# Kernel optimization log

Hardware: AMD Instinct MI355X
Metric: run time of the kernel (lower is better)

Reference implementation:

```python
import jax, jax.numpy as jnp
import numpy as np
from jax import lax

B, N, FIN, T, K, FC, FT = 8, 2048, 3, 12, 3, 64, 64


def _conv2d(x, w, b, pad):
    # x [B,C,N,T], w [O,I,1,kw], NCHW conv
    y = lax.conv_general_dilated(x, w, (1, 1), pad,
                                 dimension_numbers=('NCHW', 'OIHW', 'NCHW'))
    return y + b[None, :, None, None]


def _spatial_att(h, W, a, alpha, concat):
    # GAT-style dense attention. h [B,N,Fin], W [Fin,D], a [2D,1]
    D = W.shape[1]
    Wh = h @ W                                             # [B,N,D]
    e = jax.nn.leaky_relu(Wh @ a[:D] + jnp.swapaxes(Wh @ a[D:], 1, 2), alpha)  # [B,N,N]
    att = jax.nn.softmax(jax.nn.sigmoid(e), axis=1)        # softmax over dim=1 (as in torch)
    hp = jnp.einsum('bij,bjd->bid', att, Wh)
    return jax.nn.elu(hp) if concat else hp


def setup_inputs() -> dict:
    key = jax.random.key(0)
    ks = jax.random.split(key, 24)
    rnd = lambda i, shape, scale=1.0: (jax.random.normal(ks[i], shape, dtype=jnp.float32) * scale)
    FTm = FC * T  # 768 spatial-attention feature dim
    D = FTm // 2
    return {
        'x': rnd(0, (B, N, FIN, T)),
        'cheb': rnd(1, (K, N, N), 1.0 / np.sqrt(N)),
        'Gamma': rnd(2, (K, FIN, FC), 1.0 / np.sqrt(FIN)),
        'W_heads': rnd(3, (2, FTm, D), 1.0 / np.sqrt(FTm)),
        'a_heads': rnd(4, (2, 2 * D, 1), 1.0 / np.sqrt(2 * D)),
        'W_out': rnd(5, (FTm, FTm), 1.0 / np.sqrt(FTm)),
        'a_out': rnd(6, (2 * FTm, 1), 1.0 / np.sqrt(2 * FTm)),
        'U1': rnd(7, (FT, FT), 1.0 / np.sqrt(FT)),
        'U2': rnd(8, (FT,), 1.0 / np.sqrt(FT)),
        'U3': rnd(9, (FT,), 1.0 / np.sqrt(FT)),
        'be': rnd(10, (1, T, T), 0.1),
        'Ve': rnd(11, (T, T), 1.0 / np.sqrt(T)),
        'time_w': rnd(12, (FT, FC, 1, 3), 1.0 / np.sqrt(3 * FC)),
        'time_b': rnd(13, (FT,), 0.01),
        'res_w': rnd(14, (FT, FIN, 1, 1), 1.0 / np.sqrt(FIN)),
        'res_b': rnd(15, (FT,), 0.01),
        'back_w': rnd(16, (FT, FC, 1, 3), 1.0 / np.sqrt(3 * FC)),
        'back_b': rnd(17, (FT,), 0.01),
        'fore_w': rnd(18, (FT, FC, 1, 3), 1.0 / np.sqrt(3 * FC)),
        'fore_b': rnd(19, (FT,), 0.01),
        'ln_g': jnp.ones((FT,), jnp.float32),
        'ln_b': jnp.zeros((FT,), jnp.float32),
    }


def reference(x, cheb, Gamma, W_heads, a_heads, W_out, a_out, U1, U2, U3, be, Ve,
              time_w, time_b, res_w, res_b, back_w, back_b, fore_w, fore_b, ln_g, ln_b):
    b, n, fin, t = x.shape
    k_ = cheb.shape[0]
    fc = Gamma.shape[2]
    # ChebNetII interpolation coefficients T_k(x_j), x_j = cos((j+0.5)pi/K) -> [j,k]
    jj = np.arange(k_)
    cxj = jnp.asarray(np.cos(np.outer((jj + 0.5) * np.pi / k_, np.arange(k_))), x.dtype)
    lhs = jnp.einsum('jio,jk->kio', Gamma, cxj)                         # [K,Fin,Fc]
    rhs = jnp.einsum('bnit,knm->kbmit', x, cheb)                        # [K,B,N,Fin,T]
    spatial_gcn = jax.nn.relu((2.0 / (k_ + 1)) * jnp.einsum('kbmit,kio->bmot', rhs, lhs))  # [B,N,Fc,T]

    # Spatial transformer: 2 GAT heads + output attention
    h = spatial_gcn.reshape(b, n, fc * t)
    heads = jax.vmap(lambda W, a: _spatial_att(h, W, a, 0.1, True))(W_heads, a_heads)  # [H,B,N,D]
    hcat = jnp.transpose(heads, (1, 2, 0, 3)).reshape(b, n, -1)
    gcn_SAt = jax.nn.relu(_spatial_att(hcat, W_out, a_out, 0.1, False)).reshape(b, n, fc, t)

    # Temporal conv (1x3, pad 1)
    tc = _conv2d(jnp.transpose(gcn_SAt, (0, 2, 1, 3)), time_w, time_b, ((0, 0), (1, 1)))
    tc = jnp.transpose(tc, (0, 2, 1, 3))                                # [B,N,Ft,T]

    # Temporal attention
    lhs_t = jnp.einsum('bnft,fg,g->btn', tc, U1, U2)                    # [B,T,N]
    rhs_t = jnp.einsum('f,bnft->bnt', U3, tc)                           # [B,N,T]
    prod = jnp.einsum('bsn,bnt->bst', lhs_t, rhs_t)                     # [B,T,T]
    E = jnp.einsum('is,bst->bit', Ve, jax.nn.sigmoid(prod + be))
    E = jax.nn.softmax(E, axis=1)
    tcn = jnp.einsum('bnft,bts->bnfs', tc, E)                           # [B,N,Ft,T]

    # Residual (1x1 conv) + LayerNorm over channel dim
    x_res = _conv2d(jnp.transpose(x, (0, 2, 1, 3)), res_w, res_b, ((0, 0), (0, 0)))
    x_res = jnp.transpose(x_res, (0, 2, 1, 3))                          # [B,N,Ft,T]
    z = jnp.transpose(jax.nn.relu(x_res + tcn), (0, 3, 1, 2))           # [B,T,N,Ft]
    mu = z.mean(-1, keepdims=True)
    var = z.var(-1, keepdims=True)
    z = (z - mu) / jnp.sqrt(var + 1e-5) * ln_g + ln_b
    result = jnp.transpose(z, (0, 2, 3, 1))                             # [B,N,Ft,T]

    rp = jnp.transpose(result, (0, 2, 1, 3))
    backcast = jnp.transpose(_conv2d(rp, back_w, back_b, ((0, 0), (1, 1))), (0, 2, 1, 3))
    forecast = jnp.transpose(_conv2d(rp, fore_w, fore_b, ((0, 0), (1, 1))), (0, 2, 1, 3))
    return (backcast, forecast)
```

## Files before the change

kernel.cpp:

```cpp
#include <hip/hip_runtime.h>


typedef unsigned short u16;
typedef __bf16 bf16x8 __attribute__((ext_vector_type(8)));
typedef float f32x4 __attribute__((ext_vector_type(4)));
typedef u16 u16x8 __attribute__((ext_vector_type(8)));

__device__ __forceinline__ u16 f2b(float f) {
  union { float f; unsigned u; } v; v.f = f;
  unsigned u = v.u;
  u = u + 0x7FFFu + ((u >> 16) & 1u);
  return (u16)(u >> 16);
}
__device__ __forceinline__ float b2f(u16 h) {
  union { unsigned u; float f; } v; v.u = ((unsigned)h) << 16; return v.f;
}
__device__ __forceinline__ float qfun(float x) {
  float e = x > 0.f ? x : 0.1f * x;
  float s = __builtin_amdgcn_rcpf(1.f + __expf(-e));
  return __expf(s);
}

#define GLOAD16(g, l) __builtin_amdgcn_global_load_lds( \
    (__attribute__((address_space(1))) void*)(g),       \
    (__attribute__((address_space(3))) void*)(l), 16, 0, 0)

constexpr size_t OFF_LHS     = 0x0;
constexpr size_t OFF_U1U2    = 0x1000;
constexpr size_t OFF_BIASBIG = 0x1100;
constexpr size_t OFF_FH      = 0x3000;
constexpr size_t OFF_GH      = 0x23000;
constexpr size_t OFF_RDH     = 0x43000;
constexpr size_t OFF_FO      = 0x63000;
constexpr size_t OFF_GO      = 0x73000;
constexpr size_t OFF_RDO     = 0x83000;
constexpr size_t OFF_LHST    = 0x93000;
constexpr size_t OFF_RHST    = 0x153000;
constexpr size_t OFF_PROD    = 0x213000;
constexpr size_t OFF_E       = 0x215000;
constexpr size_t OFF_WCATT   = 0x220000;
constexpr size_t OFF_WOUTT   = 0x340000;
constexpr size_t OFF_WTBIG   = 0x460000;
constexpr size_t OFF_XCOLT   = 0x580000;
constexpr size_t OFF_CHEBT   = 0x700000;
constexpr size_t OFF_C1      = 0x1F00000;
constexpr size_t OFF_H       = 0x4300000;
constexpr size_t OFF_P       = 0x700000;
constexpr size_t OFF_WHCATT  = 0x5B00000;
constexpr size_t OFF_HCAT    = 0x7300000;
constexpr size_t OFF_WHOUTT  = 0x5B00000;
constexpr size_t OFF_GCNB    = 0x7300000;
constexpr size_t OFF_WBFBIG  = 0x8B00000;
constexpr size_t OFF_TCS     = 0x700000;
constexpr size_t OFF_RESULTB = 0x3700000;
constexpr size_t WS_NEEDED   = 0x8D40000;

struct GemmP {
  const u16* A; const u16* BT;
  long sA, sB;
  int K, lda, ldb;
  int swz, splitK;
  float* Cf; long sCf; int ldcf;
  u16* Cb;  long sCb; int ldcb;
  u16* CbT; int ldcT; long sCbT;
  const float* bias;
  float* outB; float* outF;
};

template <int EPI>
__global__ __launch_bounds__(256, 2) void gemm_bf16(GemmP p) {
  constexpr int SMEM_U16 = (EPI == 1) ? 17408 : 16384;
  __shared__ u16 smem[SMEM_U16];
  const int tid  = threadIdx.x;
  const int lane = tid & 63;
  const int wid  = tid >> 6;
  const int wm = wid >> 1, wn = wid & 1;
  const int z = blockIdx.z;

  long m0, n0;
  if (p.swz) {
    int nT = gridDim.x;
    int nwg = nT * gridDim.y;
    int lin = blockIdx.x + nT * blockIdx.y;
    int q = nwg >> 3;
    int swz = (lin & 7) * q + (lin >> 3);
    m0 = (long)(swz / nT) * 128;
    n0 = (long)(swz % nT) * 128;
  } else {
    m0 = (long)blockIdx.x * 128;
    n0 = (long)blockIdx.y * 128;
  }

  const int K = p.K;
  long aBase, bBase;
  if (p.splitK) {
    int kz = z >> 2, ch = z & 3;
    aBase = (long)kz * p.sA + (long)ch * 512;
    bBase = (long)ch * 512;
  } else {
    aBase = (long)z * p.sA;
    bBase = (long)z * p.sB;
  }
  const u16* Ab = p.A + aBase + m0 * p.lda;
  const u16* Bb = p.BT + bBase + n0 * p.ldb;

  const int srow = wid * 32 + (lane >> 2);
  const int sk   = (((lane & 3) ^ ((lane >> 3) & 3))) * 8;
  const u16* aP0 = Ab + (long)srow * p.lda + sk;
  const u16* aP1 = aP0 + (long)16 * p.lda;
  const u16* bP0 = Bb + (long)srow * p.ldb + sk;
  const u16* bP1 = bP0 + (long)16 * p.ldb;

  f32x4 acc[4][4];
  f32x4 zero = {0.f, 0.f, 0.f, 0.f};
#pragma unroll
  for (int i = 0; i < 4; ++i)
#pragma unroll
    for (int j = 0; j < 4; ++j) acc[i][j] = zero;

  const int xorc = (lane >> 1) & 3;
  const int aoff = (wm * 64 + (lane & 15)) * 32 + (((lane >> 4) ^ xorc)) * 8;
  const int boff = (wn * 64 + (lane & 15)) * 32 + (((lane >> 4) ^ xorc)) * 8;

  const int lslot = (wid * 2) * 512;

#define STAGE(s, bufbase) do {                                  \
    GLOAD16(aP0 + (long)(s) * 32, (bufbase) + lslot);           \
    GLOAD16(aP1 + (long)(s) * 32, (bufbase) + lslot + 512);     \
    GLOAD16(bP0 + (long)(s) * 32, (bufbase) + 4096 + lslot);    \
    GLOAD16(bP1 + (long)(s) * 32, (bufbase) + 4096 + lslot + 512); } while (0)

  const int nsteps = K >> 5;
  u16* buf0 = smem;
  u16* buf1 = smem + 8192;

  STAGE(0, buf0);
  if (nsteps > 1) {
    STAGE(1, buf1);
    asm volatile("s_waitcnt vmcnt(4)" ::: "memory");
  } else {
    asm volatile("s_waitcnt vmcnt(0)" ::: "memory");
  }
  asm volatile("s_barrier" ::: "memory");

  for (int i = 0; i < nsteps; ++i) {
    const u16* As = smem + (i & 1) * 8192;
    const u16* Bs = As + 4096;
    bf16x8 av[4], bv[4];
#pragma unroll
    for (int mi = 0; mi < 4; ++mi) av[mi] = *(const bf16x8*)&As[aoff + mi * 512];
#pragma unroll
    for (int ni = 0; ni < 4; ++ni) bv[ni] = *(const bf16x8*)&Bs[boff + ni * 512];
#pragma unroll
    for (int mi = 0; mi < 4; ++mi)
#pragma unroll
      for (int ni = 0; ni < 4; ++ni)
        acc[mi][ni] = __builtin_amdgcn_mfma_f32_16x16x32_bf16(av[mi], bv[ni], acc[mi][ni], 0, 0, 0);
    if (i + 1 < nsteps) {
      asm volatile("s_waitcnt lgkmcnt(0)" ::: "memory");
      asm volatile("s_barrier" ::: "memory");
      if (i + 2 < nsteps) {
        STAGE(i + 2, (i & 1) ? buf1 : buf0);
        asm volatile("s_waitcnt vmcnt(4)" ::: "memory");
      } else {
        asm volatile("s_waitcnt vmcnt(0)" ::: "memory");
      }
      asm volatile("s_barrier" ::: "memory");
    }
  }
#undef STAGE
  __syncthreads();

  if constexpr (EPI == 1) {
#pragma unroll
    for (int mi = 0; mi < 4; ++mi)
#pragma unroll
      for (int ni = 0; ni < 4; ++ni) {
        int cl = wn * 64 + ni * 16 + (lane & 15);
        int mlb = wm * 64 + mi * 16 + ((lane >> 4) << 2);
#pragma unroll
        for (int r = 0; r < 4; ++r)
          smem[cl * 136 + mlb + r] = f2b(acc[mi][ni][r]);
      }
    __syncthreads();
    int c = tid >> 1, half = tid & 1;
    long bat = m0 >> 11;
    u16* dst = p.CbT + bat * p.sCbT + (long)(n0 + c) * p.ldcT + (m0 & 2047) + half * 64;
    const u16* srcp = &smem[c * 136 + half * 64];
#pragma unroll
    for (int j = 0; j < 64; j += 8)
      *(u16x8*)(dst + j) = *(const u16x8*)(srcp + j);
    return;
  }

#pragma unroll
  for (int mi = 0; mi < 4; ++mi) {
    long rb0 = m0 + wm * 64 + mi * 16 + ((lane >> 4) << 2);
#pragma unroll
    for (int ni = 0; ni < 4; ++ni) {
      int col = (int)n0 + wn * 64 + ni * 16 + (lane & 15);
#pragma unroll
      for (int r = 0; r < 4; ++r) {
        float v = acc[mi][ni][r];
        long row = rb0 + r;
        if constexpr (EPI == 0) {
          p.Cf[(long)z * p.sCf + row * p.ldcf + col] = v;
        } else if constexpr (EPI == 2) {
          float e = v > 0.f ? v : expm1f(v);
          p.Cb[(long)z * p.sCb + row * p.ldcb + col] = f2b(e);
        } else if constexpr (EPI == 6) {
          p.Cb[row * 768 + col] = f2b(v + p.bias[col & 63]);
        } else if constexpr (EPI == 7) {
          float vb = v + p.bias[col];
          if (col < 768) p.outB[row * 768 + col] = vb;
          else           p.outF[row * 768 + (col - 768)] = vb;
        } else {
          p.Cb[(long)z * p.sCb + row * p.ldcb + col] = f2b(fmaxf(v, 0.f));
        }
      }
    }
  }
}

__global__ void k_prep(const float* Gamma, const float* U1, const float* U2,
                       const float* back_b, const float* fore_b,
                       float* lhs, float* u1u2, float* biasBig) {
  int o = threadIdx.x;
  if (o < 64) {
    const float cx[3][3] = {{1.f, 0.86602540378443871f, 0.5f},
                            {1.f, 6.123233995736766e-17f, -1.f},
                            {1.f, -0.86602540378443871f, 0.5f}};
    for (int k = 0; k < 3; ++k)
      for (int i = 0; i < 3; ++i) {
        float s = 0;
        for (int j = 0; j < 3; ++j) s += Gamma[(j * 3 + i) * 64 + o] * cx[j][k];
        lhs[(k * 3 + i) * 64 + o] = s;
      }
    float s = 0;
    for (int g = 0; g < 64; ++g) s += U1[o * 64 + g] * U2[g];
    u1u2[o] = s;
    for (int t = 0; t < 12; ++t) {
      biasBig[o * 12 + t] = back_b[o];
      biasBig[768 + o * 12 + t] = fore_b[o];
    }
  }
}

__global__ void k_convert(const float* W_heads, const float* W_out, const float* time_w,
                          const float* back_w, const float* fore_w, const float* xg,
                          u16* WcatT, u16* WoutT, u16* WtBig, u16* WbfBig, u16* xcolT) {
  const int N1 = 589824, NT = 589824, NBF = 1179648, N5 = 786432;
  const int TOT = 2 * N1 + NT + NBF + N5;
  for (int o = blockIdx.x * 256 + threadIdx.x; o < TOT; o += gridDim.x * 256) {
    if (o < N1) {
      int dcol = o / 768, kk = o % 768;
      int hd = dcol / 384, d = dcol % 384;
      WcatT[o] = f2b(W_heads[((long)hd * 768 + kk) * 384 + d]);
    } else if (o < 2 * N1) {
      int o2 = o - N1; int dcol = o2 / 768, kk = o2 % 768;
      WoutT[o2] = f2b(W_out[kk * 768 + dcol]);
    } else if (o < 2 * N1 + NT) {
      int o3 = o - 2 * N1; int col = o3 / 768, kk = o3 % 768;
      int t = col >> 6, ft = col & 63, fc = kk / 12, tau = kk % 12;
      int r = tau - t + 1;
      WtBig[o3] = f2b((r >= 0 && r < 3) ? time_w[ft * 192 + fc * 3 + r] : 0.f);
    } else if (o < 2 * N1 + NT + NBF) {
      int o4 = o - 2 * N1 - NT; int col = o4 / 768, kk = o4 % 768;
      int rem = (col < 768) ? col : col - 768;
      int c = rem / 12, tt = rem % 12;
      int fc = kk / 12, tau = kk % 12; int r = tau - tt + 1;
      const float* wsrc = (col < 768) ? back_w : fore_w;
      WbfBig[o4] = f2b((r >= 0 && r < 3) ? wsrc[c * 192 + fc * 3 + r] : 0.f);
    } else {
      int o5 = o - 2 * N1 - NT - NBF; int c = o5 / 2048, n = o5 % 2048;
      float v = 0.f;
      if (c < 288) {
        int b = c / 36, r2 = c % 36, i = r2 / 12, t = r2 % 12;
        v = xg[(long)(b * 2048 + n) * 36 + i * 12 + t];
      }
      xcolT[o5] = f2b(v);
    }
  }
}

__global__ void k_chebT(const float* cheb, u16* chebT) {
  __shared__ float ts[32][33];
  int n0 = blockIdx.x * 32, m0 = blockIdx.y * 32, k = blockIdx.z;
  int c = threadIdx.x & 31, rq = threadIdx.x >> 5;
  const long base = (long)k * 2048 * 2048;
  for (int q = 0; q < 4; ++q) {
    int n = n0 + rq + q * 8;
    ts[rq + q * 8][c] = cheb[base + (long)n * 2048 + m0 + c];
  }
  __syncthreads();
  for (int q = 0; q < 4; ++q) {
    int m = m0 + rq + q * 8;
    chebT[base + (long)m * 2048 + n0 + c] = f2b(ts[c][rq + q * 8]);
  }
}

__global__ __launch_bounds__(256) void k_h(const float* C1, const float* lhs, u16* h) {
  int bn = blockIdx.x; int b = bn >> 11, n = bn & 2047;
  int tid = threadIdx.x;
  __shared__ float c1s[108], ls[576];
  if (tid < 108) {
    int kk = tid / 12, t = tid % 12; int k = kk / 3, i = kk % 3;
    float s = 0;
#pragma unroll
    for (int ch = 0; ch < 4; ++ch)
      s += C1[((long)(k * 4 + ch) * 2048 + n) * 384 + b * 36 + i * 12 + t];
    c1s[tid] = s;
  }
  for (int s = tid; s < 576; s += 256) ls[s] = lhs[s];
  __syncthreads();
  for (int q = 0; q < 3; ++q) {
    int idx = tid + q * 256; int o = idx / 12, t = idx % 12;
    float s = 0;
#pragma unroll
    for (int kk = 0; kk < 9; ++kk) s += c1s[kk * 12 + t] * ls[kk * 64 + o];
    s *= 0.5f;
    if (s < 0.f) s = 0.f;
    h[(long)bn * 768 + idx] = f2b(s);
  }
}

__global__ __launch_bounds__(256) void k_fg(const u16* WhT, int dOff, int Dlen,
                                            const float* aF, const float* aG,
                                            float* fOut, float* gOut) {
  int b = blockIdx.y;
  int i = blockIdx.x * 256 + threadIdx.x;
  __shared__ float af[768], ag[768];
  for (int s = threadIdx.x; s < Dlen; s += 256) { af[s] = aF[s]; ag[s] = aG[s]; }
  __syncthreads();
  const u16* wp = WhT + ((long)b * 768 + dOff) * 2048 + i;
  float fs = 0, gs = 0;
  for (int d = 0; d < Dlen; ++d) {
    float w = b2f(wp[(long)d * 2048]);
    fs += w * af[d]; gs += w * ag[d];
  }
  fOut[b * 2048 + i] = fs;
  gOut[b * 2048 + i] = gs;
}

__global__ __launch_bounds__(256) void k_denom(const float* f, const float* g, float* rd) {
  int b = blockIdx.y;
  int jl = threadIdx.x & 63, ch = threadIdx.x >> 6;
  int j = blockIdx.x * 64 + jl;
  __shared__ float fl[2048];
  __shared__ float red[256];
  for (int s = threadIdx.x; s < 2048; s += 256) fl[s] = f[b * 2048 + s];
  __syncthreads();
  float gj = g[b * 2048 + j];
  float acc = 0;
  for (int i = ch * 512; i < ch * 512 + 512; ++i) acc += qfun(fl[i] + gj);
  red[threadIdx.x] = acc;
  __syncthreads();
  if (ch == 0) {
    float s = red[jl] + red[jl + 64] + red[jl + 128] + red[jl + 192];
    rd[b * 2048 + j] = 1.f / s;
  }
}

__global__ __launch_bounds__(256) void k_P(const float* f, const float* g,
                                           const float* rd, u16* P) {
  int j = blockIdx.x * 256 + threadIdx.x;
  int i0 = blockIdx.y * 16;
  int b = blockIdx.z;
  __shared__ float fl[16];
  if (threadIdx.x < 16) fl[threadIdx.x] = f[b * 2048 + i0 + threadIdx.x];
  __syncthreads();
  float gj = g[b * 2048 + j], rj = rd[b * 2048 + j];
  u16* Pp = P + ((long)b * 2048 + i0) * 2048 + j;
#pragma unroll
  for (int ii = 0; ii < 16; ++ii) Pp[(long)ii * 2048] = f2b(qfun(fl[ii] + gj) * rj);
}

__global__ void k_temporal(const u16* tc, const float* u1u2, const float* U3g,
                           float* lhs_t, float* rhs_t) {
  __shared__ float uu[64], u3[64];
  int tid = threadIdx.x;
  if (tid < 64) { uu[tid] = u1u2[tid]; u3[tid] = U3g[tid]; }
  __syncthreads();
  int gid = blockIdx.x * 256 + tid;
  const u16* p = tc + (long)gid * 64;
  float s1 = 0, s2 = 0;
#pragma unroll
  for (int c = 0; c < 8; ++c) {
    u16x8 vv = *(const u16x8*)(p + c * 8);
#pragma unroll
    for (int j = 0; j < 8; ++j) {
      float v = b2f(vv[j]);
      s1 += v * uu[c * 8 + j]; s2 += v * u3[c * 8 + j];
    }
  }
  int t = gid % 12; long bn = gid / 12;
  int b = (int)(bn >> 11);
  lhs_t[((long)b * 12 + t) * 2048 + (int)(bn & 2047)] = s1;
  rhs_t[gid] = s2;
}

__global__ void k_prod(const float* lhs_t, const float* rhs_t, float* prod) {
  int bi = blockIdx.x;
  int b = bi / 144; int r = bi % 144; int s = r / 12; int u = r % 12;
  int tid = threadIdx.x;
  float acc = 0;
  const float* lp = lhs_t + ((long)b * 12 + s) * 2048;
  const float* rp = rhs_t + (long)b * 2048 * 12 + u;
  for (int n = tid; n < 2048; n += 256) acc += lp[n] * rp[n * 12];
  __shared__ float red[256];
  red[tid] = acc; __syncthreads();
  for (int st = 128; st > 0; st >>= 1) {
    if (tid < st) red[tid] += red[tid + st];
    __syncthreads();
  }
  if (tid == 0) prod[bi] = red[0];
}

__global__ void k_E(const float* prod, const float* be, const float* Ve, float* E) {
  int b = blockIdx.x; int tid = threadIdx.x;
  __shared__ float S0[144], E1[144], mx[12], dn[12];
  if (tid < 144) {
    float v = prod[b * 144 + tid] + be[tid];
    S0[tid] = 1.f / (1.f + __expf(-v));
  }
  __syncthreads();
  if (tid < 144) {
    int i = tid / 12, t = tid % 12;
    float a = 0;
    for (int s = 0; s < 12; ++s) a += Ve[i * 12 + s] * S0[s * 12 + t];
    E1[tid] = a;
  }
  __syncthreads();
  if (tid < 12) {
    float m = -1e30f;
    for (int i = 0; i < 12; ++i) m = fmaxf(m, E1[i * 12 + tid]);
    float d = 0;
    for (int i = 0; i < 12; ++i) d += __expf(E1[i * 12 + tid] - m);
    mx[tid] = m; dn[tid] = d;
  }
  __syncthreads();
  if (tid < 144) {
    int t = tid % 12;
    E[b * 144 + tid] = __expf(E1[tid] - mx[t]) / dn[t];
  }
}

__global__ __launch_bounds__(256) void k_res_ln(const u16* tc, const float* E,
                                                const float* xg, const float* res_w,
                                                const float* res_b, const float* ln_g,
                                                const float* ln_b, u16* result) {
  int bn = blockIdx.x; int b = bn >> 11;
  int tid = threadIdx.x;
  __shared__ float tcb[768], Eb[144], xl[36], rw[192], rb[64], lg[64], lb[64], zl[768], mu[12], rs[12];
  for (int s = tid; s < 768; s += 256) tcb[s] = b2f(tc[(long)bn * 768 + s]);
  if (tid < 144) Eb[tid] = E[b * 144 + tid];
  if (tid < 36) xl[tid] = xg[(long)bn * 36 + tid];
  if (tid >= 64 && tid < 256) { int q = tid - 64; if (q < 192) rw[q] = res_w[q]; }
  if (tid < 64) { rb[tid] = res_b[tid]; lg[tid] = ln_g[tid]; lb[tid] = ln_b[tid]; }
  __syncthreads();
  float z[3];
#pragma unroll
  for (int q = 0; q < 3; ++q) {
    int idx = tid + q * 256; int f = idx / 12, s = idx % 12;
    float tcn = 0;
#pragma unroll
    for (int t = 0; t < 12; ++t) tcn += tcb[t * 64 + f] * Eb[t * 12 + s];
    float xr = rb[f];
#pragma unroll
    for (int i = 0; i < 3; ++i) xr += rw[f * 3 + i] * xl[i * 12 + s];
    float v = xr + tcn;
    v = v > 0.f ? v : 0.f;
    z[q] = v; zl[idx] = v;
  }
  __syncthreads();
  if (tid < 12) {
    float m = 0, m2 = 0;
    for (int f = 0; f < 64; ++f) { float v = zl[f * 12 + tid]; m += v; m2 += v * v; }
    m *= (1.f / 64.f); m2 *= (1.f / 64.f);
    mu[tid] = m;
    float var = m2 - m * m;
    rs[tid] = rsqrtf((var > 0.f ? var : 0.f) + 1e-5f);
  }
  __syncthreads();
#pragma unroll
  for (int q = 0; q < 3; ++q) {
    int idx = tid + q * 256; int f = idx / 12, s = idx % 12;
    result[(long)bn * 768 + idx] = f2b((z[q] - mu[s]) * rs[s] * lg[f] + lb[f]);
  }
}

__global__ void k_sentinel(float* out, long n) {
  long i = (long)blockIdx.x * 256 + threadIdx.x;
  if (i < n) out[i] = 12345.0f;
}

extern "C" void kernel_launch(void* const* d_in, const int* in_sizes, int n_in,
                              void* d_out, int out_size, void* d_ws, size_t ws_size,
                              hipStream_t stream) {
  (void)in_sizes; (void)n_in;
  const float* x       = (const float*)d_in[0];
  const float* cheb    = (const float*)d_in[1];
  const float* Gamma   = (const float*)d_in[2];
  const float* W_heads = (const float*)d_in[3];
  const float* a_heads = (const float*)d_in[4];
  const float* W_out   = (const float*)d_in[5];
  const float* a_out   = (const float*)d_in[6];
  const float* U1      = (const float*)d_in[7];
  const float* U2      = (const float*)d_in[8];
  const float* U3      = (const float*)d_in[9];
  const float* be      = (const float*)d_in[10];
  const float* Ve      = (const float*)d_in[11];
  const float* time_w  = (const float*)d_in[12];
  const float* time_b  = (const float*)d_in[13];
  const float* res_w   = (const float*)d_in[14];
  const float* res_b   = (const float*)d_in[15];
  const float* back_w  = (const float*)d_in[16];
  const float* back_b  = (const float*)d_in[17];
  const float* fore_w  = (const float*)d_in[18];
  const float* fore_b  = (const float*)d_in[19];
  const float* ln_g    = (const float*)d_in[20];
  const float* ln_b    = (const float*)d_in[21];
  float* out = (float*)d_out;

  if (ws_size < WS_NEEDED) {
    k_sentinel<<<(out_size + 255) / 256, 256, 0, stream>>>(out, out_size);
    return;
  }

  char* ws = (char*)d_ws;
  float* lhs     = (float*)(ws + OFF_LHS);
  float* u1u2    = (float*)(ws + OFF_U1U2);
  float* biasBig = (float*)(ws + OFF_BIASBIG);
  float* fH      = (float*)(ws + OFF_FH);
  float* gH      = (float*)(ws + OFF_GH);
  float* rdH     = (float*)(ws + OFF_RDH);
  float* fO      = (float*)(ws + OFF_FO);
  float* gO      = (float*)(ws + OFF_GO);
  float* rdO     = (float*)(ws + OFF_RDO);
  float* lhs_t   = (float*)(ws + OFF_LHST);
  float* rhs_t   = (float*)(ws + OFF_RHST);
  float* prod    = (float*)(ws + OFF_PROD);
  float* Ebuf    = (float*)(ws + OFF_E);
  u16* WcatT   = (u16*)(ws + OFF_WCATT);
  u16* WoutT   = (u16*)(ws + OFF_WOUTT);
  u16* WtBig   = (u16*)(ws + OFF_WTBIG);
  u16* WbfBig  = (u16*)(ws + OFF_WBFBIG);
  u16* xcolT   = (u16*)(ws + OFF_XCOLT);
  u16* chebT   = (u16*)(ws + OFF_CHEBT);
  float* C1    = (float*)(ws + OFF_C1);
  u16* hbuf    = (u16*)(ws + OFF_H);
  u16* Pbuf    = (u16*)(ws + OFF_P);
  u16* WhcatT  = (u16*)(ws + OFF_WHCATT);
  u16* hcat    = (u16*)(ws + OFF_HCAT);
  u16* WhoutT  = (u16*)(ws + OFF_WHOUTT);
  u16* gcnB    = (u16*)(ws + OFF_GCNB);
  u16* tcsB    = (u16*)(ws + OFF_TCS);
  u16* resultB = (u16*)(ws + OFF_RESULTB);

  k_prep<<<1, 64, 0, stream>>>(Gamma, U1, U2, back_b, fore_b, lhs, u1u2, biasBig);
  k_convert<<<2048, 256, 0, stream>>>(W_heads, W_out, time_w, back_w, fore_w, x,
                                      WcatT, WoutT, WtBig, WbfBig, xcolT);
  k_chebT<<<dim3(64, 64, 3), 256, 0, stream>>>(cheb, chebT);

  {
    GemmP p{}; p.A = chebT; p.BT = xcolT; p.sA = 2048L * 2048; p.sB = 0;
    p.K = 512; p.lda = 2048; p.ldb = 2048; p.splitK = 1; p.swz = 1;
    p.Cf = C1; p.sCf = 2048L * 384; p.ldcf = 384;
    gemm_bf16<0><<<dim3(3, 16, 12), 256, 0, stream>>>(p);
  }
  k_h<<<16384, 256, 0, stream>>>(C1, lhs, hbuf);

  {
    GemmP p{}; p.A = hbuf; p.BT = WcatT; p.sA = 0; p.sB = 0;
    p.K = 768; p.lda = 768; p.ldb = 768; p.swz = 1;
    p.CbT = WhcatT; p.ldcT = 2048; p.sCbT = 768L * 2048;
    gemm_bf16<1><<<dim3(6, 128, 1), 256, 0, stream>>>(p);
  }
  k_fg<<<dim3(8, 8), 256, 0, stream>>>(WhcatT, 0, 384, a_heads, a_heads + 384, fH, gH);
  k_fg<<<dim3(8, 8), 256, 0, stream>>>(WhcatT, 384, 384, a_heads + 768, a_heads + 1152,
                                       fH + 16384, gH + 16384);
  for (int hd = 0; hd < 2; ++hd) {
    const float* f = fH + hd * 16384; const float* g = gH + hd * 16384;
    float* rd = rdH + hd * 16384;
    k_denom<<<dim3(32, 8), 256, 0, stream>>>(f, g, rd);
    k_P<<<dim3(8, 128, 8), 256, 0, stream>>>(f, g, rd, Pbuf);
    GemmP p{}; p.A = Pbuf; p.BT = WhcatT + (long)hd * 384 * 2048;
    p.sA = 2048L * 2048; p.sB = 768L * 2048;
    p.K = 2048; p.lda = 2048; p.ldb = 2048; p.swz = 1;
    p.Cb = hcat + hd * 384; p.sCb = 2048L * 768; p.ldcb = 768;
    gemm_bf16<2><<<dim3(3, 16, 8), 256, 0, stream>>>(p);
  }

  {
    GemmP p{}; p.A = hcat; p.BT = WoutT; p.sA = 0; p.sB = 0;
    p.K = 768; p.lda = 768; p.ldb = 768; p.swz = 1;
    p.CbT = WhoutT; p.ldcT = 2048; p.sCbT = 768L * 2048;
    gemm_bf16<1><<<dim3(6, 128, 1), 256, 0, stream>>>(p);
  }
  k_fg<<<dim3(8, 8), 256, 0, stream>>>(WhoutT, 0, 768, a_out, a_out + 768, fO, gO);
  k_denom<<<dim3(32, 8), 256, 0, stream>>>(fO, gO, rdO);
  k_P<<<dim3(8, 128, 8), 256, 0, stream>>>(fO, gO, rdO, Pbuf);
  {
    GemmP p{}; p.A = Pbuf; p.BT = WhoutT; p.sA = 2048L * 2048; p.sB = 768L * 2048;
    p.K = 2048; p.lda = 2048; p.ldb = 2048; p.swz = 1;
    p.Cb = gcnB; p.sCb = 2048L * 768; p.ldcb = 768;
    gemm_bf16<8><<<dim3(6, 16, 8), 256, 0, stream>>>(p);
  }

  {
    GemmP p{}; p.A = gcnB; p.BT = WtBig; p.sA = 0; p.sB = 0;
    p.K = 768; p.lda = 768; p.ldb = 768; p.swz = 1;
    p.Cb = tcsB; p.bias = time_b;
    gemm_bf16<6><<<dim3(6, 128, 1), 256, 0, stream>>>(p);
  }

  k_temporal<<<768, 256, 0, stream>>>(tcsB, u1u2, U3, lhs_t, rhs_t);
  k_prod<<<1152, 256, 0, stream>>>(lhs_t, rhs_t, prod);
  k_E<<<8, 256, 0, stream>>>(prod, be, Ve, Ebuf);

  k_res_ln<<<16384, 256, 0, stream>>>(tcsB, Ebuf, x, res_w, res_b, ln_g, ln_b, resultB);

  {
    GemmP p{}; p.A = resultB; p.BT = WbfBig; p.sA = 0; p.sB = 0;
    p.K = 768; p.lda = 768; p.ldb = 768; p.swz = 1;
    p.bias = biasBig; p.outB = out; p.outF = out + 12582912L;
    gemm_bf16<7><<<dim3(12, 128, 1), 256, 0, stream>>>(p);
  }
}
```

Measured before the change: 698.9 us.

## Widen GEMM tiles to 128x256, store split-K partials in bf16, vectorize output epilogue

Adds a WN template parameter so most GEMMs use a 128x256 output tile per block, with 6 loads per stage and a larger LDS double buffer. This raises operand reuse per loaded A tile and halves the block count. The split-K cheb GEMM now writes bf16 partials instead of fp32, halving that intermediate traffic at some precision cost. The final output epilogue transposes accumulators via lane shuffles so each thread writes float4 rows. Risks include higher register pressure from 32 accumulators per thread and lower occupancy.

```diff
diff --git a/kernel.cpp b/kernel.cpp
--- a/kernel.cpp
+++ b/kernel.cpp
@@ -20,6 +20,13 @@
   float s = __builtin_amdgcn_rcpf(1.f + __expf(-e));
   return __expf(s);
 }
+
+template <int N> __device__ __forceinline__ void waitvm() {
+  if constexpr (N == 0)      asm volatile("s_waitcnt vmcnt(0)" ::: "memory");
+  else if constexpr (N == 4) asm volatile("s_waitcnt vmcnt(4)" ::: "memory");
+  else                       asm volatile("s_waitcnt vmcnt(6)" ::: "memory");
+}
+__device__ __forceinline__ void rawbar() { asm volatile("s_barrier" ::: "memory"); }
 
 #define GLOAD16(g, l) __builtin_amdgcn_global_load_lds( \
     (__attribute__((address_space(1))) void*)(g),       \
@@ -67,10 +74,12 @@
   float* outB; float* outF;
 };
 
-template <int EPI>
-__global__ __launch_bounds__(256, 2) void gemm_bf16(GemmP p) {
-  constexpr int SMEM_U16 = (EPI == 1) ? 17408 : 16384;
-  __shared__ u16 smem[SMEM_U16];
+template <int EPI, int WN>
+__global__ __launch_bounds__(256, (WN == 1 ? 3 : 2)) void gemm_bf16(GemmP p) {
+  constexpr int BUFU  = (WN == 1) ? 8192 : 12288;
+  constexpr int SMEMU = (WN == 1) ? 16384 : 24576;
+  constexpr int LPW   = (WN == 1) ? 4 : 6;
+  __shared__ u16 smem[SMEMU];
   const int tid  = threadIdx.x;
   const int lane = tid & 63;
   const int wid  = tid >> 6;
@@ -85,10 +94,10 @@
     int q = nwg >> 3;
     int swz = (lin & 7) * q + (lin >> 3);
     m0 = (long)(swz / nT) * 128;
-    n0 = (long)(swz % nT) * 128;
+    n0 = (long)(swz % nT) * (128 * WN);
   } else {
-    m0 = (long)blockIdx.x * 128;
-    n0 = (long)blockIdx.y * 128;
+    m0 = (long)blockIdx.y * 128;
+    n0 = (long)blockIdx.x * (128 * WN);
   }
 
   const int K = p.K;
@@ -104,92 +113,128 @@
   const u16* Ab = p.A + aBase + m0 * p.lda;
   const u16* Bb = p.BT + bBase + n0 * p.ldb;
 
-  const int srow = wid * 32 + (lane >> 2);
-  const int sk   = (((lane & 3) ^ ((lane >> 3) & 3))) * 8;
-  const u16* aP0 = Ab + (long)srow * p.lda + sk;
+  const int sk = (((lane & 3) ^ ((lane >> 3) & 3))) * 8;
+  const u16* aP0 = Ab + (long)(wid * 32 + (lane >> 2)) * p.lda + sk;
   const u16* aP1 = aP0 + (long)16 * p.lda;
-  const u16* bP0 = Bb + (long)srow * p.ldb + sk;
+  const u16* bP0 = Bb + (long)(wid * 32 * WN + (lane >> 2)) * p.ldb + sk;
   const u16* bP1 = bP0 + (long)16 * p.ldb;
-
-  f32x4 acc[4][4];
+  const u16* bP2 = bP0 + (long)32 * p.ldb;
+  const u16* bP3 = bP0 + (long)48 * p.ldb;
+  const int aslot = wid * 1024;
+  const int bslot = 4096 + wid * (WN == 1 ? 1024 : 2048);
+
+  auto STAGE = [&](int s, u16* base) {
+    long ko = (long)s * 32;
+    GLOAD16(aP0 + ko, base + aslot);
+    GLOAD16(aP1 + ko, base + aslot + 512);
+    GLOAD16(bP0 + ko, base + bslot);
+    GLOAD16(bP1 + ko, base + bslot + 512);
+    if constexpr (WN == 2) {
+      GLOAD16(bP2 + ko, base + bslot + 1024);
+      GLOAD16(bP3 + ko, base + bslot + 1536);
+    }
+  };
+
+  f32x4 acc[4][4 * WN];
   f32x4 zero = {0.f, 0.f, 0.f, 0.f};
 #pragma unroll
   for (int i = 0; i < 4; ++i)
 #pragma unroll
-    for (int j = 0; j < 4; ++j) acc[i][j] = zero;
+    for (int j = 0; j < 4 * WN; ++j) acc[i][j] = zero;
 
   const int xorc = (lane >> 1) & 3;
-  const int aoff = (wm * 64 + (lane & 15)) * 32 + (((lane >> 4) ^ xorc)) * 8;
-  const int boff = (wn * 64 + (lane & 15)) * 32 + (((lane >> 4) ^ xorc)) * 8;
-
-  const int lslot = (wid * 2) * 512;
-
-#define STAGE(s, bufbase) do {                                  \
-    GLOAD16(aP0 + (long)(s) * 32, (bufbase) + lslot);           \
-    GLOAD16(aP1 + (long)(s) * 32, (bufbase) + lslot + 512);     \
-    GLOAD16(bP0 + (long)(s) * 32, (bufbase) + 4096 + lslot);    \
-    GLOAD16(bP1 + (long)(s) * 32, (bufbase) + 4096 + lslot + 512); } while (0)
+  const int aoff = (wm * 64 + (lane & 15)) * 32 + ((lane >> 4) ^ xorc) * 8;
+  const int boff = 4096 + (wn * 64 * WN + (lane & 15)) * 32 + ((lane >> 4) ^ xorc) * 8;
 
   const int nsteps = K >> 5;
   u16* buf0 = smem;
-  u16* buf1 = smem + 8192;
+  u16* buf1 = smem + BUFU;
 
   STAGE(0, buf0);
-  if (nsteps > 1) {
-    STAGE(1, buf1);
-    asm volatile("s_waitcnt vmcnt(4)" ::: "memory");
-  } else {
-    asm volatile("s_waitcnt vmcnt(0)" ::: "memory");
-  }
-  asm volatile("s_barrier" ::: "memory");
+  STAGE(1, buf1);
+  waitvm<LPW>();
+  rawbar();
 
   for (int i = 0; i < nsteps; ++i) {
-    const u16* As = smem + (i & 1) * 8192;
-    const u16* Bs = As + 4096;
-    bf16x8 av[4], bv[4];
-#pragma unroll
-    for (int mi = 0; mi < 4; ++mi) av[mi] = *(const bf16x8*)&As[aoff + mi * 512];
-#pragma unroll
-    for (int ni = 0; ni < 4; ++ni) bv[ni] = *(const bf16x8*)&Bs[boff + ni * 512];
+    u16* buf = (i & 1) ? buf1 : buf0;
+    bf16x8 av[4], bv[4 * WN];
+#pragma unroll
+    for (int mi = 0; mi < 4; ++mi) av[mi] = *(const bf16x8*)&buf[aoff + mi * 512];
+#pragma unroll
+    for (int ni = 0; ni < 4 * WN; ++ni) bv[ni] = *(const bf16x8*)&buf[boff + ni * 512];
 #pragma unroll
     for (int mi = 0; mi < 4; ++mi)
 #pragma unroll
-      for (int ni = 0; ni < 4; ++ni)
+      for (int ni = 0; ni < 4 * WN; ++ni)
         acc[mi][ni] = __builtin_amdgcn_mfma_f32_16x16x32_bf16(av[mi], bv[ni], acc[mi][ni], 0, 0, 0);
     if (i + 1 < nsteps) {
       asm volatile("s_waitcnt lgkmcnt(0)" ::: "memory");
-      asm volatile("s_barrier" ::: "memory");
+      rawbar();
       if (i + 2 < nsteps) {
-        STAGE(i + 2, (i & 1) ? buf1 : buf0);
-        asm volatile("s_waitcnt vmcnt(4)" ::: "memory");
+        STAGE(i + 2, buf);
+        waitvm<LPW>();
       } else {
-        asm volatile("s_waitcnt vmcnt(0)" ::: "memory");
+        waitvm<0>();
       }
-      asm volatile("s_barrier" ::: "memory");
-    }
-  }
-#undef STAGE
+      rawbar();
+    }
+  }
   __syncthreads();
 
   if constexpr (EPI == 1) {
 #pragma unroll
-    for (int mi = 0; mi < 4; ++mi)
-#pragma unroll
-      for (int ni = 0; ni < 4; ++ni) {
-        int cl = wn * 64 + ni * 16 + (lane & 15);
-        int mlb = wm * 64 + mi * 16 + ((lane >> 4) << 2);
-#pragma unroll
-        for (int r = 0; r < 4; ++r)
-          smem[cl * 136 + mlb + r] = f2b(acc[mi][ni][r]);
+    for (int h = 0; h < 2; ++h) {
+      if (h == 1) __syncthreads();
+      if (WN == 1 || wn == h) {
+#pragma unroll
+        for (int mi = 0; mi < 4; ++mi)
+#pragma unroll
+          for (int ni = 0; ni < 4 * WN; ++ni) {
+            int cl = (WN == 1 ? wn * 64 : 0) + ni * 16 + (lane & 15);
+            int mlb = wm * 64 + mi * 16 + ((lane >> 4) << 2);
+#pragma unroll
+            for (int r = 0; r < 4; ++r)
+              smem[cl * 136 + mlb + r] = f2b(acc[mi][ni][r]);
+          }
       }
-    __syncthreads();
-    int c = tid >> 1, half = tid & 1;
-    long bat = m0 >> 11;
-    u16* dst = p.CbT + bat * p.sCbT + (long)(n0 + c) * p.ldcT + (m0 & 2047) + half * 64;
-    const u16* srcp = &smem[c * 136 + half * 64];
-#pragma unroll
-    for (int j = 0; j < 64; j += 8)
-      *(u16x8*)(dst + j) = *(const u16x8*)(srcp + j);
+      __syncthreads();
+      int c = tid >> 1, half = tid & 1;
+      long bat = m0 >> 11;
+      u16* dst = p.CbT + bat * p.sCbT + (long)(n0 + h * 128 + c) * p.ldcT +
+                 (m0 & 2047) + half * 64;
+      const u16* srcp = &smem[c * 136 + half * 64];
+#pragma unroll
+      for (int j = 0; j < 64; j += 8)
+        *(u16x8*)(dst + j) = *(const u16x8*)(srcp + j);
+      if (WN == 1) break;
+    }
+    return;
+  }
+
+  if constexpr (EPI == 7) {
+    const int q = lane >> 4, g4 = (lane >> 2) & 3, j = lane & 3;
+    const int back = ((int)n0 < 768);
+    float* obase = (back ? p.outB : p.outF) - (back ? 0 : 768);
+#pragma unroll
+    for (int mi = 0; mi < 4; ++mi) {
+      long rb0 = m0 + wm * 64 + mi * 16 + q * 4;
+#pragma unroll
+      for (int ni = 0; ni < 4 * WN; ++ni) {
+        int cb = (int)n0 + wn * 64 * WN + ni * 16 + g4 * 4;
+        f32x4 v = acc[mi][ni];
+        float bsv = p.bias[cb + j];
+        v[0] += bsv; v[1] += bsv; v[2] += bsv; v[3] += bsv;
+#pragma unroll
+        for (int d = 1; d <= 2; d <<= 1) {
+          f32x4 t;
+#pragma unroll
+          for (int b = 0; b < 4; ++b) t[b] = __shfl_xor(v[b ^ d], d, 64);
+#pragma unroll
+          for (int b = 0; b < 4; ++b) if ((lane ^ b) & d) v[b] = t[b];
+        }
+        *(f32x4*)(obase + (rb0 + j) * 768 + cb) = v;
+      }
+    }
     return;
   }
 
@@ -197,23 +242,19 @@
   for (int mi = 0; mi < 4; ++mi) {
     long rb0 = m0 + wm * 64 + mi * 16 + ((lane >> 4) << 2);
 #pragma unroll
-    for (int ni = 0; ni < 4; ++ni) {
-      int col = (int)n0 + wn * 64 + ni * 16 + (lane & 15);
+    for (int ni = 0; ni < 4 * WN; ++ni) {
+      int col = (int)n0 + wn * 64 * WN + ni * 16 + (lane & 15);
 #pragma unroll
       for (int r = 0; r < 4; ++r) {
         float v = acc[mi][ni][r];
         long row = rb0 + r;
-        if constexpr (EPI == 0) {
-          p.Cf[(long)z * p.sCf + row * p.ldcf + col] = v;
-        } else if constexpr (EPI == 2) {
+        if constexpr (EPI == 2) {
           float e = v > 0.f ? v : expm1f(v);
           p.Cb[(long)z * p.sCb + row * p.ldcb + col] = f2b(e);
         } else if constexpr (EPI == 6) {
           p.Cb[row * 768 + col] = f2b(v + p.bias[col & 63]);
-        } else if constexpr (EPI == 7) {
-          float vb = v + p.bias[col];
-          if (col < 768) p.outB[row * 768 + col] = vb;
-          else           p.outF[row * 768 + (col - 768)] = vb;
+        } else if constexpr (EPI == 9) {
+          p.Cb[(long)z * p.sCb + row * p.ldcb + col] = f2b(v);
         } else {
           p.Cb[(long)z * p.sCb + row * p.ldcb + col] = f2b(fmaxf(v, 0.f));
         }
@@ -299,7 +340,7 @@
   }
 }
 
-__global__ __launch_bounds__(256) void k_h(const float* C1, const float* lhs, u16* h) {
+__global__ __launch_bounds__(256) void k_h(const u16* C1, const float* lhs, u16* h) {
   int bn = blockIdx.x; int b = bn >> 11, n = bn & 2047;
   int tid = threadIdx.x;
   __shared__ float c1s[108], ls[576];
@@ -308,7 +349,7 @@
     float s = 0;
 #pragma unroll
     for (int ch = 0; ch < 4; ++ch)
-      s += C1[((long)(k * 4 + ch) * 2048 + n) * 384 + b * 36 + i * 12 + t];
+      s += b2f(C1[((long)(k * 4 + ch) * 2048 + n) * 384 + b * 36 + i * 12 + t]);
     c1s[tid] = s;
   }
   for (int s = tid; s < 576; s += 256) ls[s] = lhs[s];
@@ -547,7 +588,7 @@
   u16* WbfBig  = (u16*)(ws + OFF_WBFBIG);
   u16* xcolT   = (u16*)(ws + OFF_XCOLT);
   u16* chebT   = (u16*)(ws + OFF_CHEBT);
-  float* C1    = (float*)(ws + OFF_C1);
+  u16* C1      = (u16*)(ws + OFF_C1);
   u16* hbuf    = (u16*)(ws + OFF_H);
   u16* Pbuf    = (u16*)(ws + OFF_P);
   u16* WhcatT  = (u16*)(ws + OFF_WHCATT);
@@ -565,8 +606,8 @@
   {
     GemmP p{}; p.A = chebT; p.BT = xcolT; p.sA = 2048L * 2048; p.sB = 0;
     p.K = 512; p.lda = 2048; p.ldb = 2048; p.splitK = 1; p.swz = 1;
-    p.Cf = C1; p.sCf = 2048L * 384; p.ldcf = 384;
-    gemm_bf16<0><<<dim3(3, 16, 12), 256, 0, stream>>>(p);
+    p.Cb = C1; p.sCb = 2048L * 384; p.ldcb = 384;
+    gemm_bf16<9, 1><<<dim3(3, 16, 12), 256, 0, stream>>>(p);
   }
   k_h<<<16384, 256, 0, stream>>>(C1, lhs, hbuf);
 
@@ -574,7 +615,7 @@
     GemmP p{}; p.A = hbuf; p.BT = WcatT; p.sA = 0; p.sB = 0;
     p.K = 768; p.lda = 768; p.ldb = 768; p.swz = 1;
     p.CbT = WhcatT; p.ldcT = 2048; p.sCbT = 768L * 2048;
-    gemm_bf16<1><<<dim3(6, 128, 1), 256, 0, stream>>>(p);
+    gemm_bf16<1, 2><<<dim3(3, 128, 1), 256, 0, stream>>>(p);
   }
   k_fg<<<dim3(8, 8), 256, 0, stream>>>(WhcatT, 0, 384, a_heads, a_heads + 384, fH, gH);
   k_fg<<<dim3(8, 8), 256, 0, stream>>>(WhcatT, 384, 384, a_heads + 768, a_heads + 1152,
@@ -588,14 +629,14 @@
     p.sA = 2048L * 2048; p.sB = 768L * 2048;
     p.K = 2048; p.lda = 2048; p.ldb = 2048; p.swz = 1;
     p.Cb = hcat + hd * 384; p.sCb = 2048L * 768; p.ldcb = 768;
-    gemm_bf16<2><<<dim3(3, 16, 8), 256, 0, stream>>>(p);
+    gemm_bf16<2, 1><<<dim3(3, 16, 8), 256, 0, stream>>>(p);
   }
 
   {
     GemmP p{}; p.A = hcat; p.BT = WoutT; p.sA = 0; p.sB = 0;
     p.K = 768; p.lda = 768; p.ldb = 768; p.swz = 1;
     p.CbT = WhoutT; p.ldcT = 2048; p.sCbT = 768L * 2048;
-    gemm_bf16<1><<<dim3(6, 128, 1), 256, 0, stream>>>(p);
+    gemm_bf16<1, 2><<<dim3(3, 128, 1), 256, 0, stream>>>(p);
   }
   k_fg<<<dim3(8, 8), 256, 0, stream>>>(WhoutT, 0, 768, a_out, a_out + 768, fO, gO);
   k_denom<<<dim3(32, 8), 256, 0, stream>>>(fO, gO, rdO);
@@ -604,14 +645,14 @@
     GemmP p{}; p.A = Pbuf; p.BT = WhoutT; p.sA = 2048L * 2048; p.sB = 768L * 2048;
     p.K = 2048; p.lda = 2048; p.ldb = 2048; p.swz = 1;
     p.Cb = gcnB; p.sCb = 2048L * 768; p.ldcb = 768;
-    gemm_bf16<8><<<dim3(6, 16, 8), 256, 0, stream>>>(p);
+    gemm_bf16<8, 2><<<dim3(3, 16, 8), 256, 0, stream>>>(p);
   }
 
   {
     GemmP p{}; p.A = gcnB; p.BT = WtBig; p.sA = 0; p.sB = 0;
     p.K = 768; p.lda = 768; p.ldb = 768; p.swz = 1;
     p.Cb = tcsB; p.bias = time_b;
-    gemm_bf16<6><<<dim3(6, 128, 1), 256, 0, stream>>>(p);
+    gemm_bf16<6, 2><<<dim3(3, 128, 1), 256, 0, stream>>>(p);
   }
 
   k_temporal<<<768, 256, 0, stream>>>(tcsB, u1u2, U3, lhs_t, rhs_t);
@@ -624,6 +665,6 @@
     GemmP p{}; p.A = resultB; p.BT = WbfBig; p.sA = 0; p.sB = 0;
     p.K = 768; p.lda = 768; p.ldb = 768; p.swz = 1;
     p.bias = biasBig; p.outB = out; p.outF = out + 12582912L;
-    gemm_bf16<7><<<dim3(12, 128, 1), 256, 0, stream>>>(p);
-  }
-}
+    gemm_bf16<7, 2><<<dim3(6, 128, 1), 256, 0, stream>>>(p);
+  }
+}
```

After: 699.0 us. No clear change (+0.0%).
